# Performance work log

Measured on AMD Instinct MI355X. Metric: run time of the kernel, lower is better.

The kernel has to match this reference:

```python
import jax, jax.numpy as jnp
import numpy as np

D_MODEL = 1024
N_HEADS = 16
HEAD_DIM = D_MODEL // N_HEADS
D_FF = 4096
ROPE_BASE = 10000.0
LN_EPS = 1e-5


def setup_inputs() -> dict:
    key = jax.random.key(0)
    ks = jax.random.split(key, 12)
    B, S = 2, 2048
    s = 0.02
    inp = {
        "x": jax.random.normal(ks[0], (B, S, D_MODEL), dtype=jnp.float32),
        "Wq": jax.random.normal(ks[1], (D_MODEL, D_MODEL), dtype=jnp.float32) * s,
        "bq": jnp.zeros((D_MODEL,), jnp.float32),
        "Wk": jax.random.normal(ks[2], (D_MODEL, D_MODEL), dtype=jnp.float32) * s,
        "bk": jnp.zeros((D_MODEL,), jnp.float32),
        "Wv": jax.random.normal(ks[3], (D_MODEL, D_MODEL), dtype=jnp.float32) * s,
        "bv": jnp.zeros((D_MODEL,), jnp.float32),
        "Wo": jax.random.normal(ks[4], (D_MODEL, D_MODEL), dtype=jnp.float32) * s,
        "bo": jnp.zeros((D_MODEL,), jnp.float32),
        "ln1_g": jnp.ones((D_MODEL,), jnp.float32),
        "ln1_b": jnp.zeros((D_MODEL,), jnp.float32),
        "W1": jax.random.normal(ks[5], (D_MODEL, D_FF), dtype=jnp.float32) * s,
        "b1": jnp.zeros((D_FF,), jnp.float32),
        "W2": jax.random.normal(ks[6], (D_FF, D_MODEL), dtype=jnp.float32) * s,
        "b2": jnp.zeros((D_MODEL,), jnp.float32),
        "ln2_g": jnp.ones((D_MODEL,), jnp.float32),
        "ln2_b": jnp.zeros((D_MODEL,), jnp.float32),
    }
    return inp


def _layernorm(x, g, b):
    mu = jnp.mean(x, axis=-1, keepdims=True)
    var = jnp.var(x, axis=-1, keepdims=True)
    return (x - mu) * jax.lax.rsqrt(var + LN_EPS) * g + b


def _rope_cos_sin(seq_len, dtype):
    inv_freq = 1.0 / (ROPE_BASE ** (jnp.arange(0, HEAD_DIM, 2, dtype=jnp.float32) / HEAD_DIM))
    t = jnp.arange(seq_len, dtype=jnp.float32)
    freqs = jnp.einsum("i,j->ij", t, inv_freq)          # [S, HEAD_DIM/2]
    emb = jnp.concatenate([freqs, freqs], axis=-1)        # [S, HEAD_DIM]
    return jnp.cos(emb).astype(dtype), jnp.sin(emb).astype(dtype)


def _rotate_half(x):
    x1, x2 = jnp.split(x, 2, axis=-1)
    return jnp.concatenate([-x2, x1], axis=-1)


def reference(x, Wq, bq, Wk, bk, Wv, bv, Wo, bo, ln1_g, ln1_b,
              W1, b1, W2, b2, ln2_g, ln2_b):
    B, S, _ = x.shape
    residual = x
    h = _layernorm(x, ln1_g, ln1_b)

    def split_heads(y):  # [B,S,D] -> [B,H,S,hd]
        return y.reshape(B, S, N_HEADS, HEAD_DIM).transpose(0, 2, 1, 3)

    q = split_heads(h @ Wq + bq)
    k = split_heads(h @ Wk + bk)
    v = split_heads(h @ Wv + bv)

    cos, sin = _rope_cos_sin(S, x.dtype)  # [S, hd], broadcast over B,H
    q = q * cos + _rotate_half(q) * sin
    k = k * cos + _rotate_half(k) * sin

    scale = HEAD_DIM ** -0.5
    scores = jnp.einsum("bhqd,bhkd->bhqk", q, k) * scale
    attn = jax.nn.softmax(scores, axis=-1)
    ctx = jnp.einsum("bhqk,bhkd->bhqd", attn, v)           # [B,H,S,hd]
    ctx = ctx.transpose(0, 2, 1, 3).reshape(B, S, D_MODEL)
    attn_out = ctx @ Wo + bo

    x = residual + attn_out
    residual = x
    h = _layernorm(x, ln2_g, ln2_b)
    ffn = jax.nn.gelu(h @ W1 + b1, approximate=False) @ W2 + b2
    return residual + ffn
```

## Files before the change

### kernel.cpp

```cpp
#include <hip/hip_runtime.h>
#include <hip/hip_bf16.h>
#include <stdint.h>

#define S_LEN 2048
#define NH 16
#define HD 64
#define DM 1024
#define DFF 4096
#define MTOK 4096

typedef __attribute__((ext_vector_type(8))) short short8;
typedef __attribute__((ext_vector_type(4))) float f32x4;
typedef __attribute__((ext_vector_type(16))) float f32x16;
typedef __attribute__((ext_vector_type(2))) int i32x2;
typedef unsigned short u16;
typedef unsigned int u32;

__device__ __forceinline__ float bf2f(u16 u) {
  union { u32 i; float f; } x; x.i = ((u32)u) << 16; return x.f;
}
__device__ __forceinline__ u16 f2bf(float f) {
  union { float f; u32 i; } x; x.f = f;
  u32 r = x.i + 0x7fffu + ((x.i >> 16) & 1u);
  return (u16)(r >> 16);
}
__device__ __forceinline__ float exp2_fast(float x) {
  union { int i; float f; } u;
  u.i = (int)__builtin_fmaf(x, 8388608.0f, 1064986823.0f);
  return u.f;
}
__device__ __forceinline__ void gload16(const u16* g, u16* l) {
  __builtin_amdgcn_global_load_lds(
      (__attribute__((address_space(1))) u32*)g,
      (__attribute__((address_space(3))) u32*)l, 16, 0, 0);
}

#define VM0 asm volatile("s_waitcnt vmcnt(0)" ::: "memory")
#define BARR do { __builtin_amdgcn_s_barrier(); asm volatile("" ::: "memory"); } while (0)
#define LGKM0 do { asm volatile("s_waitcnt lgkmcnt(0)" ::: "memory"); __builtin_amdgcn_sched_barrier(0); } while (0)
#define PRIO1 __builtin_amdgcn_s_setprio(1)
#define PRIO0 __builtin_amdgcn_s_setprio(0)

__device__ __forceinline__ void transpose_tile(const float* __restrict__ W,
                                               u16* __restrict__ Wt, int K, int N,
                                               int n0, int k0, int tx, int ty,
                                               float (*tile)[33]) {
#pragma unroll
  for (int i = 0; i < 4; ++i)
    tile[ty + i * 8][tx] = W[(size_t)(k0 + ty + i * 8) * N + n0 + tx];
  __syncthreads();
#pragma unroll
  for (int i = 0; i < 4; ++i)
    Wt[(size_t)(n0 + ty + i * 8) * K + k0 + tx] = f2bf(tile[tx][ty + i * 8]);
}

__global__ __launch_bounds__(256) void prep(
    const float* __restrict__ Wq, const float* __restrict__ Wk,
    const float* __restrict__ Wv, const float* __restrict__ Wo,
    const float* __restrict__ W1, const float* __restrict__ W2,
    u16* __restrict__ WQKVT, u16* __restrict__ WOT, u16* __restrict__ W1T,
    u16* __restrict__ W2T, float* __restrict__ cosT, float* __restrict__ sinT,
    const float* __restrict__ x, const float* __restrict__ g,
    const float* __restrict__ b, u16* __restrict__ H) {
  __shared__ float tile[32][33];
  __shared__ float red[8];
  const int r = blockIdx.x;
  const int t = threadIdx.x;
  const int tx = t & 31, ty = t >> 5;
  if (r < 4096) {
    const float* W = (r < 1024) ? Wq : (r < 2048) ? Wk : (r < 3072) ? Wv : Wo;
    u16* Wt = (r < 1024) ? WQKVT
              : (r < 2048) ? WQKVT + 1024 * 1024
              : (r < 3072) ? WQKVT + 2 * 1024 * 1024 : WOT;
    int sub = r & 1023;
    transpose_tile(W, Wt, 1024, 1024, (sub & 31) * 32, (sub >> 5) * 32, tx, ty, tile);
  } else if (r < 8192) {
    int sub = r - 4096;
    transpose_tile(W1, W1T, 1024, 4096, (sub & 127) * 32, (sub >> 7) * 32, tx, ty, tile);
  } else if (r < 12288) {
    int sub = r - 8192;
    transpose_tile(W2, W2T, 4096, 1024, (sub & 31) * 32, (sub >> 5) * 32, tx, ty, tile);
  } else if (r < 12544) {
    int id = (r - 12288) * 256 + t;
    int s = id >> 5, j = id & 31;
    float inv = powf(10000.0f, -(float)j * (1.0f / 32.0f));
    float fr = (float)s * inv;
    cosT[id] = cosf(fr);
    sinT[id] = sinf(fr);
  } else {
    int row = r - 12544;
    float4 v = ((const float4*)(x + ((size_t)row << 10)))[t];
    float s = v.x + v.y + v.z + v.w;
    float q = v.x * v.x + v.y * v.y + v.z * v.z + v.w * v.w;
#pragma unroll
    for (int m = 1; m < 64; m <<= 1) {
      s += __shfl_xor(s, m, 64);
      q += __shfl_xor(q, m, 64);
    }
    int lane = t & 63, w = t >> 6;
    if (lane == 0) { red[w] = s; red[4 + w] = q; }
    __syncthreads();
    s = red[0] + red[1] + red[2] + red[3];
    q = red[4] + red[5] + red[6] + red[7];
    float mu = s * (1.0f / 1024.0f);
    float var = q * (1.0f / 1024.0f) - mu * mu;
    float rstd = rsqrtf(var + 1e-5f);
    float4 gv = ((const float4*)g)[t];
    float4 bv = ((const float4*)b)[t];
    ushort4 o;
    o.x = f2bf((v.x - mu) * rstd * gv.x + bv.x);
    o.y = f2bf((v.y - mu) * rstd * gv.y + bv.y);
    o.z = f2bf((v.z - mu) * rstd * gv.z + bv.z);
    o.w = f2bf((v.w - mu) * rstd * gv.w + bv.w);
    ((ushort4*)(H + ((size_t)row << 10)))[t] = o;
  }
}

__global__ __launch_bounds__(256) void ln_bf16(const float* __restrict__ x,
                                               const float* __restrict__ g,
                                               const float* __restrict__ b,
                                               u16* __restrict__ out) {
  int row = blockIdx.x;
  int t = threadIdx.x;
  float4 v = ((const float4*)(x + ((size_t)row << 10)))[t];
  float s = v.x + v.y + v.z + v.w;
  float q = v.x * v.x + v.y * v.y + v.z * v.z + v.w * v.w;
#pragma unroll
  for (int m = 1; m < 64; m <<= 1) {
    s += __shfl_xor(s, m, 64);
    q += __shfl_xor(q, m, 64);
  }
  __shared__ float red[8];
  int lane = t & 63, w = t >> 6;
  if (lane == 0) { red[w] = s; red[4 + w] = q; }
  __syncthreads();
  s = red[0] + red[1] + red[2] + red[3];
  q = red[4] + red[5] + red[6] + red[7];
  float mu = s * (1.0f / 1024.0f);
  float var = q * (1.0f / 1024.0f) - mu * mu;
  float rstd = rsqrtf(var + 1e-5f);
  float4 gv = ((const float4*)g)[t];
  float4 bv = ((const float4*)b)[t];
  ushort4 o;
  o.x = f2bf((v.x - mu) * rstd * gv.x + bv.x);
  o.y = f2bf((v.y - mu) * rstd * gv.y + bv.y);
  o.z = f2bf((v.z - mu) * rstd * gv.z + bv.z);
  o.w = f2bf((v.w - mu) * rstd * gv.w + bv.w);
  ((ushort4*)(out + ((size_t)row << 10)))[t] = o;
}

#define MMQ(IB, NB)                                                          \
  _Pragma("unroll") for (int i_ = 0; i_ < 4; ++i_)                           \
  _Pragma("unroll") for (int n_ = 0; n_ < 2; ++n_)                           \
  _Pragma("unroll") for (int k_ = 0; k_ < 2; ++k_)                           \
    acc[(IB) + i_][(NB) + n_] = __builtin_amdgcn_mfma_f32_16x16x32_bf16(     \
        a[i_][k_], b[(NB) + n_][k_], acc[(IB) + i_][(NB) + n_], 0, 0, 0);

template <int EPI>
__global__ __launch_bounds__(512, 2) void gemm256(
    const u16* __restrict__ A, const u16* __restrict__ Bt, int N, int K,
    const float* __restrict__ bias, const float* __restrict__ bq,
    const float* __restrict__ bk, const float* __restrict__ bv,
    const float* __restrict__ cosT, const float* __restrict__ sinT,
    u16* __restrict__ d0, u16* __restrict__ d1, u16* __restrict__ d2) {
  __shared__ __align__(16) u16 As[2][256 * 64];
  __shared__ __align__(16) u16 Bs[2][256 * 64];
  const int t = threadIdx.x;
  const int lane = t & 63, wid = t >> 6;
  const int fr = lane & 15, fq = lane >> 4;
  const int m0 = blockIdx.y << 8, n0 = blockIdx.x << 8;
  const int wmo = (wid >> 2) << 7;
  const int wno = (wid & 3) << 6;
  const int r7 = fr & 7;
  const int srow = t >> 3, ssl = t & 7;

  f32x4 acc[8][4];
#pragma unroll
  for (int i = 0; i < 8; ++i)
#pragma unroll
    for (int n = 0; n < 4; ++n) acc[i][n] = (f32x4){0.f, 0.f, 0.f, 0.f};

  short8 a[4][2], b[4][2];

  auto stageA = [&](int slot, int kt) {
#pragma unroll
    for (int c = 0; c < 4; ++c) {
      const int row = (c << 6) + srow;
      gload16(A + (size_t)(m0 + row) * K + kt + ((ssl ^ (row & 7)) << 3),
              &As[slot][(size_t)((c << 9) + t) << 3]);
    }
  };
  auto stageB = [&](int slot, int kt) {
#pragma unroll
    for (int c = 0; c < 4; ++c) {
      const int row = (c << 6) + srow;
      gload16(Bt + (size_t)(n0 + row) * K + kt + ((ssl ^ (row & 7)) << 3),
              &Bs[slot][(size_t)((c << 9) + t) << 3]);
    }
  };
  auto readA = [&](int slot, int ibase) {
#pragma unroll
    for (int i = 0; i < 4; ++i) {
      const u16* rp = &As[slot][(wmo + ((ibase + i) << 4) + fr) << 6];
      a[i][0] = *(const short8*)(rp + ((fq ^ r7) << 3));
      a[i][1] = *(const short8*)(rp + (((4 + fq) ^ r7) << 3));
    }
  };
  auto readB = [&](int slot, int nbase) {
#pragma unroll
    for (int n = 0; n < 2; ++n) {
      const u16* rp = &Bs[slot][(wno + ((nbase + n) << 4) + fr) << 6];
      b[nbase + n][0] = *(const short8*)(rp + ((fq ^ r7) << 3));
      b[nbase + n][1] = *(const short8*)(rp + (((4 + fq) ^ r7) << 3));
    }
  };

  stageA(0, 0);
  stageB(0, 0);
  const int iters = K >> 7;
  for (int it = 0; it < iters; ++it) {
    const int kt = it << 7;
    VM0; BARR;
    readA(0, 0); readB(0, 0);
    stageA(1, kt + 64);
    LGKM0; PRIO1; MMQ(0, 0); PRIO0;
    BARR;
    readB(0, 2);
    stageB(1, kt + 64);
    LGKM0; PRIO1; MMQ(0, 2); PRIO0;
    BARR;
    readA(0, 4);
    LGKM0; PRIO1; MMQ(4, 2); PRIO0;
    BARR;
    PRIO1; MMQ(4, 0); PRIO0;
    VM0; BARR;
    readA(1, 0); readB(1, 0);
    if (it + 1 < iters) stageA(0, kt + 128);
    LGKM0; PRIO1; MMQ(0, 0); PRIO0;
    BARR;
    readB(1, 2);
    if (it + 1 < iters) stageB(0, kt + 128);
    LGKM0; PRIO1; MMQ(0, 2); PRIO0;
    BARR;
    readA(1, 4);
    LGKM0; PRIO1; MMQ(4, 2); PRIO0;
    BARR;
    PRIO1; MMQ(4, 0); PRIO0;
  }

  if (EPI == 0) {
    const int colbase = n0 + wno;
    const int slice = colbase >> 10;
    const int cb = colbase & 1023;
    const int hh = cb >> 6;
    if (slice < 2) {
      const float sc = (slice == 0) ? 0.125f * 1.44269504088896f : 1.0f;
      const float* bb_ = (slice == 0) ? bq : bk;
      u16* dst = (slice == 0) ? d0 : d1;
#pragma unroll
      for (int i = 0; i < 8; ++i) {
        const int row0 = m0 + wmo + (i << 4) + (fq << 2);
#pragma unroll
        for (int n = 0; n < 2; ++n) {
          const int d = n * 16 + fr;
          const float blo = bb_[cb + d];
          const float bhi = bb_[cb + d + 32];
#pragma unroll
          for (int j = 0; j < 4; ++j) {
            const int row = row0 + j;
            const int ss = row & 2047, bb2 = row >> 11;
            const float c = cosT[ss * 32 + d];
            const float sn = sinT[ss * 32 + d];
            const float av = acc[i][n][j] + blo;
            const float bv2 = acc[i][n + 2][j] + bhi;
            const size_t base = ((size_t)((bb2 * 16 + hh) * 2048 + ss)) << 6;
            dst[base + d] = f2bf((av * c - bv2 * sn) * sc);
            dst[base + d + 32] = f2bf((bv2 * c + av * sn) * sc);
          }
        }
      }
    } else {
#pragma unroll
      for (int i = 0; i < 8; ++i) {
        const int row0 = m0 + wmo + (i << 4) + (fq << 2);
#pragma unroll
        for (int n = 0; n < 4; ++n) {
          const int d = n * 16 + fr;
          const float bia = bv[cb + d];
#pragma unroll
          for (int j = 0; j < 4; ++j) {
            const int row = row0 + j;
            const int ss = row & 2047, bb2 = row >> 11;
            d2[((size_t)((bb2 * 16 + hh) * 64 + d)) * 2048 + ss] =
                f2bf(acc[i][n][j] + bia);
          }
        }
      }
    }
  } else {
#pragma unroll
    for (int i = 0; i < 8; ++i) {
      const int row0 = m0 + wmo + (i << 4) + (fq << 2);
#pragma unroll
      for (int n = 0; n < 4; ++n) {
        const int col = n0 + wno + n * 16 + fr;
        const float bia = bias[col];
#pragma unroll
        for (int j = 0; j < 4; ++j) {
          const int row = row0 + j;
          const float v = acc[i][n][j] + bia;
          const float gl = 0.5f * v * (1.0f + erff(v * 0.70710678118f));
          d0[(size_t)row * N + col] = f2bf(gl);
        }
      }
    }
  }
}

__global__ __launch_bounds__(512, 1) void gemm_split(
    const u16* __restrict__ A, const u16* __restrict__ Bt, int K,
    const float* __restrict__ bias, const float* __restrict__ resid,
    float* __restrict__ dst) {
  __shared__ __align__(16) u16 As[2][128 * 128];
  __shared__ __align__(16) u16 Bs[2][128 * 128];
  const int t = threadIdx.x, lane = t & 63, w = t >> 6;
  const int fr = lane & 15, fq = lane >> 4;
  const int wq = w & 3, kh = w >> 2;
  const int wm = (wq >> 1) << 6, wn = (wq & 1) << 6;
  const int bid = blockIdx.x;
  const int xcd = bid & 7, within = bid >> 3;
  const int m0 = (xcd * 4 + (within >> 3)) << 7;
  const int n0 = (within & 7) << 7;
  const int srow = t >> 4;
  const int ssl = t & 15;

  f32x4 acc[4][4];
#pragma unroll
  for (int i = 0; i < 4; ++i)
#pragma unroll
    for (int n = 0; n < 4; ++n) acc[i][n] = (f32x4){0.f, 0.f, 0.f, 0.f};

  auto stage = [&](int buf, int kt) {
#pragma unroll
    for (int c = 0; c < 4; ++c) {
      const int R = c * 32 + srow;
      const int gs = ssl ^ (R & 15);
      gload16(A + (size_t)(m0 + R) * K + kt + gs * 8, &As[buf][R * 128 + ssl * 8]);
    }
#pragma unroll
    for (int c = 0; c < 4; ++c) {
      const int R = c * 32 + srow;
      const int gs = ssl ^ (R & 15);
      gload16(Bt + (size_t)(n0 + R) * K + kt + gs * 8, &Bs[buf][R * 128 + ssl * 8]);
    }
  };

  stage(0, 0);
  int buf = 0;
  const int iters = K >> 7;
  for (int it = 0; it < iters; ++it) {
    VM0;
    BARR;
    if (it + 1 < iters) stage(buf ^ 1, (it + 1) << 7);

    short8 a[4][2], b[4][2];
#pragma unroll
    for (int i = 0; i < 4; ++i) {
      const u16* rp = &As[buf][(wm + i * 16 + fr) * 128];
#pragma unroll
      for (int ks = 0; ks < 2; ++ks)
        a[i][ks] = *(const short8*)(rp + (((kh * 8 + ks * 4 + fq) ^ fr) << 3));
    }
#pragma unroll
    for (int n = 0; n < 4; ++n) {
      const u16* rp = &Bs[buf][(wn + n * 16 + fr) * 128];
#pragma unroll
      for (int ks = 0; ks < 2; ++ks)
        b[n][ks] = *(const short8*)(rp + (((kh * 8 + ks * 4 + fq) ^ fr) << 3));
    }
    PRIO1;
#pragma unroll
    for (int i = 0; i < 4; ++i)
#pragma unroll
      for (int n = 0; n < 4; ++n)
#pragma unroll
        for (int ks = 0; ks < 2; ++ks)
          acc[i][n] = __builtin_amdgcn_mfma_f32_16x16x32_bf16(a[i][ks], b[n][ks],
                                                              acc[i][n], 0, 0, 0);
    PRIO0;
    buf ^= 1;
  }

  BARR;
  float* mrg = (float*)&As[0][0];
  if (kh == 1) {
#pragma unroll
    for (int i = 0; i < 4; ++i) {
      const int ri = i * 16 + (fq << 2);
#pragma unroll
      for (int n = 0; n < 4; ++n) {
        const int ci = n * 16 + fr;
        *(f32x4*)(mrg + wq * 4352 + ci * 68 + ri) = acc[i][n];
      }
    }
  }
  LGKM0;
  BARR;
  if (kh == 0) {
#pragma unroll
    for (int i = 0; i < 4; ++i) {
      const int ri = i * 16 + (fq << 2);
      const int row0 = m0 + wm + ri;
#pragma unroll
      for (int n = 0; n < 4; ++n) {
        const int ci = n * 16 + fr;
        const int col = n0 + wn + ci;
        const f32x4 other = *(const f32x4*)(mrg + wq * 4352 + ci * 68 + ri);
        const float bia = bias[col];
#pragma unroll
        for (int j = 0; j < 4; ++j) {
          size_t idx = (size_t)(row0 + j) * 1024 + col;
          dst[idx] = acc[i][n][j] + other[j] + bia + resid[idx];
        }
      }
    }
  }
}

__global__ __launch_bounds__(512, 4) void attn_fwd(const u16* __restrict__ q,
                                                   const u16* __restrict__ k,
                                                   const u16* __restrict__ vt,
                                                   u16* __restrict__ ctx) {
  __shared__ __align__(16) u16 Ks[2][2][64 * 64];
  __shared__ __align__(16) u16 Vs[2][2][64 * 64];
  __shared__ float Lr[4][32];
  const int t = threadIdx.x, lane = t & 63, w = t >> 6;
  const int qsub = w & 3, half = w >> 2;
  const int ql = lane & 31;
  const int h = lane >> 5;
  const int bid = blockIdx.x;
  const int bh = (bid & 7) * 4 + ((bid >> 3) & 3);
  const int qt = bid >> 5;
  const int q0w = qt * 128 + qsub * 32;
  const size_t hbase = (size_t)bh << 17;
  const u16* kg = k + hbase;
  const u16* vg = vt + hbase;
  const int srow = t >> 3;
  const int sl = t & 7;
  const int l7 = lane & 7;

  short8 qf[4];
#pragma unroll
  for (int f = 0; f < 4; ++f)
    qf[f] = *(const short8*)(q + hbase + (size_t)(q0w + ql) * 64 + f * 16 + h * 8);

  float la[4] = {0.f, 0.f, 0.f, 0.f};
  f32x16 o[2];
#pragma unroll
  for (int db = 0; db < 2; ++db)
#pragma unroll
    for (int r = 0; r < 16; ++r) o[db][r] = 0.f;

  auto stage = [&](int buf, int it1) {
    const int kt0 = it1 << 6;
    const int kt1 = (16 + it1) << 6;
    const int gs = sl ^ (srow & 7);
    gload16(kg + (size_t)(kt0 + srow) * 64 + gs * 8, &Ks[0][buf][srow * 64 + sl * 8]);
    gload16(kg + (size_t)(kt1 + srow) * 64 + gs * 8, &Ks[1][buf][srow * 64 + sl * 8]);
    gload16(vg + (size_t)srow * 2048 + kt0 + gs * 8, &Vs[0][buf][srow * 64 + sl * 8]);
    gload16(vg + (size_t)srow * 2048 + kt1 + gs * 8, &Vs[1][buf][srow * 64 + sl * 8]);
  };

  stage(0, 0);
  int buf = 0;
  for (int it = 0; it < 16; ++it) {
    VM0;
    BARR;
    if (it < 15) stage(buf ^ 1, it + 1);

    f32x16 s[2];
    PRIO1;
#pragma unroll
    for (int kb = 0; kb < 2; ++kb) {
#pragma unroll
      for (int r = 0; r < 16; ++r) s[kb][r] = 0.f;
#pragma unroll
      for (int f = 0; f < 4; ++f) {
        const u16* kr = &Ks[half][buf][(kb * 32 + ql) * 64 + (((2 * f + h) ^ l7) << 3)];
        s[kb] = __builtin_amdgcn_mfma_f32_32x32x16_bf16(*(const short8*)kr, qf[f],
                                                        s[kb], 0, 0, 0);
      }
    }
    PRIO0;

    float p[2][16];
#pragma unroll
    for (int kb = 0; kb < 2; ++kb)
#pragma unroll
      for (int r = 0; r < 16; ++r) {
        p[kb][r] = exp2_fast(s[kb][r]);
        la[r & 3] += p[kb][r];
      }

    short8 pf[4];
#pragma unroll
    for (int kb = 0; kb < 2; ++kb)
#pragma unroll
      for (int rrp = 0; rrp < 2; ++rrp) {
        u32 y0, y1, x0, x1;
        asm volatile("v_cvt_pk_bf16_f32 %0, %1, %2" : "=v"(y0)
                     : "v"(p[kb][8 * rrp + 0]), "v"(p[kb][8 * rrp + 1]));
        asm volatile("v_cvt_pk_bf16_f32 %0, %1, %2" : "=v"(y1)
                     : "v"(p[kb][8 * rrp + 2]), "v"(p[kb][8 * rrp + 3]));
        asm volatile("v_cvt_pk_bf16_f32 %0, %1, %2" : "=v"(x0)
                     : "v"(p[kb][8 * rrp + 4]), "v"(p[kb][8 * rrp + 5]));
        asm volatile("v_cvt_pk_bf16_f32 %0, %1, %2" : "=v"(x1)
                     : "v"(p[kb][8 * rrp + 6]), "v"(p[kb][8 * rrp + 7]));
        i32x2 r0 = __builtin_amdgcn_permlane32_swap((int)x0, (int)y0, false, false);
        i32x2 r1 = __builtin_amdgcn_permlane32_swap((int)x1, (int)y1, false, false);
        u32 dw[4] = {(u32)r0[1], (u32)r1[1], (u32)r0[0], (u32)r1[0]};
        pf[kb * 2 + rrp] = *(short8*)dw;
      }

    PRIO1;
#pragma unroll
    for (int db = 0; db < 2; ++db) {
#pragma unroll
      for (int f = 0; f < 4; ++f) {
        const u16* vr = &Vs[half][buf][(db * 32 + ql) * 64 + (((2 * f + h) ^ l7) << 3)];
        o[db] = __builtin_amdgcn_mfma_f32_32x32x16_bf16(pf[f], *(const short8*)vr,
                                                        o[db], 0, 0, 0);
      }
    }
    PRIO0;
    buf ^= 1;
  }

  float lacc = (la[0] + la[1]) + (la[2] + la[3]);
  lacc += __shfl_xor(lacc, 32, 64);

  BARR;
  float* mO = (float*)&Ks[0][0][0];
  float* mL = (float*)&Vs[0][0][0];
  if (half == 1) {
#pragma unroll
    for (int r = 0; r < 16; ++r) {
      const int qr = (r & 3) + 8 * (r >> 2) + 4 * h;
#pragma unroll
      for (int db = 0; db < 2; ++db)
        mO[(qsub * 32 + qr) * 64 + db * 32 + ql] = o[db][r];
    }
    if (h == 0) mL[qsub * 32 + ql] = lacc;
  }
  LGKM0;
  BARR;
  if (half == 0) {
    float lsum = lacc + mL[qsub * 32 + ql];
    Lr[qsub][ql] = 1.0f / lsum;
#pragma unroll
    for (int r = 0; r < 16; ++r) {
      const int qr = (r & 3) + 8 * (r >> 2) + 4 * h;
#pragma unroll
      for (int db = 0; db < 2; ++db)
        o[db][r] += mO[(qsub * 32 + qr) * 64 + db * 32 + ql];
    }
    LGKM0;
    const int bb = bh >> 4, hh = bh & 15;
#pragma unroll
    for (int r = 0; r < 16; ++r) {
      const int qr = (r & 3) + 8 * (r >> 2) + 4 * h;
      const float rl = Lr[qsub][qr];
      const int row = q0w + qr;
      const size_t base = (((size_t)(bb * 2048 + row)) << 10) + hh * 64;
#pragma unroll
      for (int db = 0; db < 2; ++db)
        ctx[base + db * 32 + ql] = f2bf(o[db][r] * rl);
    }
  }
}

extern "C" void kernel_launch(void* const* d_in, const int* in_sizes, int n_in,
                              void* d_out, int out_size, void* d_ws, size_t ws_size,
                              hipStream_t stream) {
  const float* x    = (const float*)d_in[0];
  const float* Wq   = (const float*)d_in[1];
  const float* bq   = (const float*)d_in[2];
  const float* Wk   = (const float*)d_in[3];
  const float* bk   = (const float*)d_in[4];
  const float* Wv   = (const float*)d_in[5];
  const float* bv   = (const float*)d_in[6];
  const float* Wo   = (const float*)d_in[7];
  const float* bo   = (const float*)d_in[8];
  const float* ln1g = (const float*)d_in[9];
  const float* ln1b = (const float*)d_in[10];
  const float* W1   = (const float*)d_in[11];
  const float* b1   = (const float*)d_in[12];
  const float* W2   = (const float*)d_in[13];
  const float* b2   = (const float*)d_in[14];
  const float* ln2g = (const float*)d_in[15];
  const float* ln2b = (const float*)d_in[16];

  char* ws = (char*)d_ws;
  size_t off = 0;
  auto alloc = [&](size_t bytes) {
    char* p = ws + off;
    off += (bytes + 1023) & ~(size_t)1023;
    return p;
  };
  u16* WQKVT = (u16*)alloc((size_t)3 * DM * DM * 2);
  u16* WOT = (u16*)alloc((size_t)DM * DM * 2);
  u16* W1T = (u16*)alloc((size_t)DFF * DM * 2);
  u16* W2T = (u16*)alloc((size_t)DM * DFF * 2);
  float* COS = (float*)alloc((size_t)S_LEN * 32 * 4);
  float* SIN = (float*)alloc((size_t)S_LEN * 32 * 4);
  u16* H   = (u16*)alloc((size_t)MTOK * DM * 2);
  u16* Qb  = (u16*)alloc((size_t)MTOK * DM * 2);
  u16* Kb  = (u16*)alloc((size_t)MTOK * DM * 2);
  u16* VT  = (u16*)alloc((size_t)MTOK * DM * 2);
  u16* CTX = (u16*)alloc((size_t)MTOK * DM * 2);
  float* X2 = (float*)alloc((size_t)MTOK * DM * 4);
  u16* FFN1 = Qb;
  if (ws_size < off) return;

  dim3 blk256(256);
  prep<<<dim3(16640), blk256, 0, stream>>>(Wq, Wk, Wv, Wo, W1, W2, WQKVT, WOT,
                                           W1T, W2T, COS, SIN, x, ln1g, ln1b, H);
  gemm256<0><<<dim3(12, 16), dim3(512), 0, stream>>>(
      H, WQKVT, 3072, 1024, nullptr, bq, bk, bv, COS, SIN, Qb, Kb, VT);
  attn_fwd<<<dim3(512), dim3(512), 0, stream>>>(Qb, Kb, VT, CTX);
  gemm_split<<<dim3(256), dim3(512), 0, stream>>>(CTX, WOT, 1024, bo, x, X2);
  ln_bf16<<<4096, blk256, 0, stream>>>(X2, ln2g, ln2b, H);
  gemm256<1><<<dim3(16, 16), dim3(512), 0, stream>>>(
      H, W1T, 4096, 1024, b1, nullptr, nullptr, nullptr, nullptr, nullptr,
      FFN1, nullptr, nullptr);
  gemm_split<<<dim3(256), dim3(512), 0, stream>>>(FFN1, W2T, 4096, b2, X2, (float*)d_out);
}
```

Baseline: 219.6 us.

## Restructure GEMM main loop into half-tile staged pipeline with partial vmcnt waits

Rewrites the 256x256 GEMM main loop so that global-to-LDS loads are issued in half-tile chunks spread across the four MFMA phases, prefetching two k-tiles ahead. A partial vmcnt(6) wait replaces the full drain. All eight A fragments are now read once per k-tile, and launch bounds drop to one block per CU so the doubled A register array fits. The aim is to hide global load latency and reduce stalls, at the cost of lower occupancy and more register pressure.

Result: no change. 220.2 us (+0.2%).

```diff
diff --git a/kernel.cpp b/kernel.cpp
--- a/kernel.cpp
+++ b/kernel.cpp
@@ -36,6 +36,7 @@
 }
 
 #define VM0 asm volatile("s_waitcnt vmcnt(0)" ::: "memory")
+#define VM6 asm volatile("s_waitcnt vmcnt(6)" ::: "memory")
 #define BARR do { __builtin_amdgcn_s_barrier(); asm volatile("" ::: "memory"); } while (0)
 #define LGKM0 do { asm volatile("s_waitcnt lgkmcnt(0)" ::: "memory"); __builtin_amdgcn_sched_barrier(0); } while (0)
 #define PRIO1 __builtin_amdgcn_s_setprio(1)
@@ -149,15 +150,15 @@
   ((ushort4*)(out + ((size_t)row << 10)))[t] = o;
 }
 
-#define MMQ(IB, NB)                                                          \
+#define MMQ4(IB, NB)                                                         \
   _Pragma("unroll") for (int i_ = 0; i_ < 4; ++i_)                           \
   _Pragma("unroll") for (int n_ = 0; n_ < 2; ++n_)                           \
   _Pragma("unroll") for (int k_ = 0; k_ < 2; ++k_)                           \
     acc[(IB) + i_][(NB) + n_] = __builtin_amdgcn_mfma_f32_16x16x32_bf16(     \
-        a[i_][k_], b[(NB) + n_][k_], acc[(IB) + i_][(NB) + n_], 0, 0, 0);
+        a[(IB) + i_][k_], b[(NB) + n_][k_], acc[(IB) + i_][(NB) + n_], 0, 0, 0);
 
 template <int EPI>
-__global__ __launch_bounds__(512, 2) void gemm256(
+__global__ __launch_bounds__(512, 1) void gemm256(
     const u16* __restrict__ A, const u16* __restrict__ Bt, int N, int K,
     const float* __restrict__ bias, const float* __restrict__ bq,
     const float* __restrict__ bk, const float* __restrict__ bv,
@@ -172,7 +173,9 @@
   const int wmo = (wid >> 2) << 7;
   const int wno = (wid & 3) << 6;
   const int r7 = fr & 7;
-  const int srow = t >> 3, ssl = t & 7;
+  const int ssl = t & 7;
+  const u16* Ap = A + (size_t)m0 * K;
+  const u16* Bp = Bt + (size_t)n0 * K;
 
   f32x4 acc[8][4];
 #pragma unroll
@@ -180,33 +183,25 @@
 #pragma unroll
     for (int n = 0; n < 4; ++n) acc[i][n] = (f32x4){0.f, 0.f, 0.f, 0.f};
 
-  short8 a[4][2], b[4][2];
-
-  auto stageA = [&](int slot, int kt) {
-#pragma unroll
-    for (int c = 0; c < 4; ++c) {
-      const int row = (c << 6) + srow;
-      gload16(A + (size_t)(m0 + row) * K + kt + ((ssl ^ (row & 7)) << 3),
-              &As[slot][(size_t)((c << 9) + t) << 3]);
+  short8 a[8][2], b[4][2];
+
+  auto stageH = [&](u16* dstSlot, const u16* src, int rowOff, int kt) {
+#pragma unroll
+    for (int c = 0; c < 2; ++c) {
+      const int R = rowOff + (c << 6) + (t >> 3);
+      gload16(src + (size_t)R * K + kt + ((ssl ^ (R & 7)) << 3),
+              dstSlot + (size_t)R * 64 + ssl * 8);
     }
   };
-  auto stageB = [&](int slot, int kt) {
-#pragma unroll
-    for (int c = 0; c < 4; ++c) {
-      const int row = (c << 6) + srow;
-      gload16(Bt + (size_t)(n0 + row) * K + kt + ((ssl ^ (row & 7)) << 3),
-              &Bs[slot][(size_t)((c << 9) + t) << 3]);
-    }
-  };
-  auto readA = [&](int slot, int ibase) {
-#pragma unroll
-    for (int i = 0; i < 4; ++i) {
-      const u16* rp = &As[slot][(wmo + ((ibase + i) << 4) + fr) << 6];
+  auto readAall = [&](int slot) {
+#pragma unroll
+    for (int i = 0; i < 8; ++i) {
+      const u16* rp = &As[slot][(wmo + (i << 4) + fr) << 6];
       a[i][0] = *(const short8*)(rp + ((fq ^ r7) << 3));
       a[i][1] = *(const short8*)(rp + (((4 + fq) ^ r7) << 3));
     }
   };
-  auto readB = [&](int slot, int nbase) {
+  auto readB2 = [&](int slot, int nbase) {
 #pragma unroll
     for (int n = 0; n < 2; ++n) {
       const u16* rp = &Bs[slot][(wno + ((nbase + n) << 4) + fr) << 6];
@@ -215,37 +210,36 @@
     }
   };
 
-  stageA(0, 0);
-  stageB(0, 0);
-  const int iters = K >> 7;
-  for (int it = 0; it < iters; ++it) {
-    const int kt = it << 7;
-    VM0; BARR;
-    readA(0, 0); readB(0, 0);
-    stageA(1, kt + 64);
-    LGKM0; PRIO1; MMQ(0, 0); PRIO0;
+  const int nt = K >> 6;
+  stageH(&As[0][0], Ap, 0, 0);
+  stageH(&As[0][0], Ap, 128, 0);
+  stageH(&Bs[0][0], Bp, 0, 0);
+  stageH(&Bs[0][0], Bp, 128, 0);
+  stageH(&As[1][0], Ap, 0, 64);
+  stageH(&As[1][0], Ap, 128, 64);
+  stageH(&Bs[1][0], Bp, 0, 64);
+
+  for (int tt = 0; tt < nt; ++tt) {
+    const int s = tt & 1;
+    const int kt1 = (tt + 1) << 6, kt2 = (tt + 2) << 6;
+    if (tt + 1 < nt) { VM6; } else { VM0; }
     BARR;
-    readB(0, 2);
-    stageB(1, kt + 64);
-    LGKM0; PRIO1; MMQ(0, 2); PRIO0;
+    readAall(s);
+    readB2(s, 0);
+    if (tt + 1 < nt) stageH(&Bs[s ^ 1][0], Bp, 128, kt1);
+    LGKM0;
+    PRIO1; MMQ4(0, 0); PRIO0;
     BARR;
-    readA(0, 4);
-    LGKM0; PRIO1; MMQ(4, 2); PRIO0;
+    readB2(s, 2);
+    if (tt + 2 < nt) stageH(&As[s][0], Ap, 0, kt2);
+    LGKM0;
+    PRIO1; MMQ4(0, 2); PRIO0;
     BARR;
-    PRIO1; MMQ(4, 0); PRIO0;
-    VM0; BARR;
-    readA(1, 0); readB(1, 0);
-    if (it + 1 < iters) stageA(0, kt + 128);
-    LGKM0; PRIO1; MMQ(0, 0); PRIO0;
+    if (tt + 2 < nt) stageH(&As[s][0], Ap, 128, kt2);
+    PRIO1; MMQ4(4, 2); PRIO0;
     BARR;
-    readB(1, 2);
-    if (it + 1 < iters) stageB(0, kt + 128);
-    LGKM0; PRIO1; MMQ(0, 2); PRIO0;
-    BARR;
-    readA(1, 4);
-    LGKM0; PRIO1; MMQ(4, 2); PRIO0;
-    BARR;
-    PRIO1; MMQ(4, 0); PRIO0;
+    if (tt + 2 < nt) stageH(&Bs[s][0], Bp, 0, kt2);
+    PRIO1; MMQ4(4, 0); PRIO0;
   }
 
   if (EPI == 0) {
```

## Replace 256x256 double-buffered GEMM with simple 128x128 single-buffered tile GEMM

Applied to the files above, without the earlier changes.

Swaps the 256x256-tile, 8-wave, double-buffered, phase-interleaved GEMM used for QKV projection and FFN1 for a 128x128-tile, 4-wave kernel with one LDS buffer and a plain sync-load-compute loop. Blocks are mapped to tiles with a swizzle to improve L2 locality. The intent is more blocks in flight: 768/1024 blocks and 3 per CU, instead of 192/256 blocks that underfill 256 CUs. The cost is losing load/compute overlap and getting lower operand reuse per tile.

Measured after the change: 216.1 us. About the same (-1.6%).

```diff
diff --git a/kernel.cpp b/kernel.cpp
--- a/kernel.cpp
+++ b/kernel.cpp
@@ -149,107 +149,71 @@
   ((ushort4*)(out + ((size_t)row << 10)))[t] = o;
 }
 
-#define MMQ(IB, NB)                                                          \
-  _Pragma("unroll") for (int i_ = 0; i_ < 4; ++i_)                           \
-  _Pragma("unroll") for (int n_ = 0; n_ < 2; ++n_)                           \
-  _Pragma("unroll") for (int k_ = 0; k_ < 2; ++k_)                           \
-    acc[(IB) + i_][(NB) + n_] = __builtin_amdgcn_mfma_f32_16x16x32_bf16(     \
-        a[i_][k_], b[(NB) + n_][k_], acc[(IB) + i_][(NB) + n_], 0, 0, 0);
-
 template <int EPI>
-__global__ __launch_bounds__(512, 2) void gemm256(
+__global__ __launch_bounds__(256, 3) void gemm128(
     const u16* __restrict__ A, const u16* __restrict__ Bt, int N, int K,
     const float* __restrict__ bias, const float* __restrict__ bq,
     const float* __restrict__ bk, const float* __restrict__ bv,
     const float* __restrict__ cosT, const float* __restrict__ sinT,
     u16* __restrict__ d0, u16* __restrict__ d1, u16* __restrict__ d2) {
-  __shared__ __align__(16) u16 As[2][256 * 64];
-  __shared__ __align__(16) u16 Bs[2][256 * 64];
+  __shared__ __align__(16) u16 As[128 * 64];
+  __shared__ __align__(16) u16 Bs[128 * 64];
   const int t = threadIdx.x;
   const int lane = t & 63, wid = t >> 6;
   const int fr = lane & 15, fq = lane >> 4;
-  const int m0 = blockIdx.y << 8, n0 = blockIdx.x << 8;
-  const int wmo = (wid >> 2) << 7;
-  const int wno = (wid & 3) << 6;
   const int r7 = fr & 7;
+  const int bid = blockIdx.x;
+  const int mt = (bid & 7) * 4 + ((bid >> 3) & 3);
+  const int ntl = bid >> 5;
+  const int m0 = mt << 7, n0 = ntl << 7;
+  const int wm = (wid >> 1) << 6, wn = (wid & 1) << 6;
   const int srow = t >> 3, ssl = t & 7;
 
-  f32x4 acc[8][4];
-#pragma unroll
-  for (int i = 0; i < 8; ++i)
+  f32x4 acc[4][4];
+#pragma unroll
+  for (int i = 0; i < 4; ++i)
 #pragma unroll
     for (int n = 0; n < 4; ++n) acc[i][n] = (f32x4){0.f, 0.f, 0.f, 0.f};
 
-  short8 a[4][2], b[4][2];
-
-  auto stageA = [&](int slot, int kt) {
+  for (int kt = 0; kt < K; kt += 64) {
+    __syncthreads();
 #pragma unroll
     for (int c = 0; c < 4; ++c) {
-      const int row = (c << 6) + srow;
-      gload16(A + (size_t)(m0 + row) * K + kt + ((ssl ^ (row & 7)) << 3),
-              &As[slot][(size_t)((c << 9) + t) << 3]);
-    }
-  };
-  auto stageB = [&](int slot, int kt) {
-#pragma unroll
-    for (int c = 0; c < 4; ++c) {
-      const int row = (c << 6) + srow;
-      gload16(Bt + (size_t)(n0 + row) * K + kt + ((ssl ^ (row & 7)) << 3),
-              &Bs[slot][(size_t)((c << 9) + t) << 3]);
-    }
-  };
-  auto readA = [&](int slot, int ibase) {
+      const int R = (c << 5) + srow;
+      const int gs = ssl ^ (R & 7);
+      gload16(A + (size_t)(m0 + R) * K + kt + gs * 8, As + R * 64 + ssl * 8);
+      gload16(Bt + (size_t)(n0 + R) * K + kt + gs * 8, Bs + R * 64 + ssl * 8);
+    }
+    __syncthreads();
+    short8 a[4][2], b[4][2];
 #pragma unroll
     for (int i = 0; i < 4; ++i) {
-      const u16* rp = &As[slot][(wmo + ((ibase + i) << 4) + fr) << 6];
-      a[i][0] = *(const short8*)(rp + ((fq ^ r7) << 3));
-      a[i][1] = *(const short8*)(rp + (((4 + fq) ^ r7) << 3));
-    }
-  };
-  auto readB = [&](int slot, int nbase) {
-#pragma unroll
-    for (int n = 0; n < 2; ++n) {
-      const u16* rp = &Bs[slot][(wno + ((nbase + n) << 4) + fr) << 6];
-      b[nbase + n][0] = *(const short8*)(rp + ((fq ^ r7) << 3));
-      b[nbase + n][1] = *(const short8*)(rp + (((4 + fq) ^ r7) << 3));
-    }
-  };
-
-  stageA(0, 0);
-  stageB(0, 0);
-  const int iters = K >> 7;
-  for (int it = 0; it < iters; ++it) {
-    const int kt = it << 7;
-    VM0; BARR;
-    readA(0, 0); readB(0, 0);
-    stageA(1, kt + 64);
-    LGKM0; PRIO1; MMQ(0, 0); PRIO0;
-    BARR;
-    readB(0, 2);
-    stageB(1, kt + 64);
-    LGKM0; PRIO1; MMQ(0, 2); PRIO0;
-    BARR;
-    readA(0, 4);
-    LGKM0; PRIO1; MMQ(4, 2); PRIO0;
-    BARR;
-    PRIO1; MMQ(4, 0); PRIO0;
-    VM0; BARR;
-    readA(1, 0); readB(1, 0);
-    if (it + 1 < iters) stageA(0, kt + 128);
-    LGKM0; PRIO1; MMQ(0, 0); PRIO0;
-    BARR;
-    readB(1, 2);
-    if (it + 1 < iters) stageB(0, kt + 128);
-    LGKM0; PRIO1; MMQ(0, 2); PRIO0;
-    BARR;
-    readA(1, 4);
-    LGKM0; PRIO1; MMQ(4, 2); PRIO0;
-    BARR;
-    PRIO1; MMQ(4, 0); PRIO0;
+      const u16* rp = &As[(wm + i * 16 + fr) * 64];
+#pragma unroll
+      for (int ks = 0; ks < 2; ++ks)
+        a[i][ks] = *(const short8*)(rp + (((ks * 4 + fq) ^ r7) << 3));
+    }
+#pragma unroll
+    for (int n = 0; n < 4; ++n) {
+      const u16* rp = &Bs[(wn + n * 16 + fr) * 64];
+#pragma unroll
+      for (int ks = 0; ks < 2; ++ks)
+        b[n][ks] = *(const short8*)(rp + (((ks * 4 + fq) ^ r7) << 3));
+    }
+    PRIO1;
+#pragma unroll
+    for (int i = 0; i < 4; ++i)
+#pragma unroll
+      for (int n = 0; n < 4; ++n)
+#pragma unroll
+        for (int ks = 0; ks < 2; ++ks)
+          acc[i][n] = __builtin_amdgcn_mfma_f32_16x16x32_bf16(a[i][ks], b[n][ks],
+                                                              acc[i][n], 0, 0, 0);
+    PRIO0;
   }
 
   if (EPI == 0) {
-    const int colbase = n0 + wno;
+    const int colbase = n0 + wn;
     const int slice = colbase >> 10;
     const int cb = colbase & 1023;
     const int hh = cb >> 6;
@@ -258,8 +222,8 @@
       const float* bb_ = (slice == 0) ? bq : bk;
       u16* dst = (slice == 0) ? d0 : d1;
 #pragma unroll
-      for (int i = 0; i < 8; ++i) {
-        const int row0 = m0 + wmo + (i << 4) + (fq << 2);
+      for (int i = 0; i < 4; ++i) {
+        const int row0 = m0 + wm + i * 16 + (fq << 2);
 #pragma unroll
         for (int n = 0; n < 2; ++n) {
           const int d = n * 16 + fr;
@@ -281,8 +245,8 @@
       }
     } else {
 #pragma unroll
-      for (int i = 0; i < 8; ++i) {
-        const int row0 = m0 + wmo + (i << 4) + (fq << 2);
+      for (int i = 0; i < 4; ++i) {
+        const int row0 = m0 + wm + i * 16 + (fq << 2);
 #pragma unroll
         for (int n = 0; n < 4; ++n) {
           const int d = n * 16 + fr;
@@ -299,11 +263,11 @@
     }
   } else {
 #pragma unroll
-    for (int i = 0; i < 8; ++i) {
-      const int row0 = m0 + wmo + (i << 4) + (fq << 2);
+    for (int i = 0; i < 4; ++i) {
+      const int row0 = m0 + wm + i * 16 + (fq << 2);
 #pragma unroll
       for (int n = 0; n < 4; ++n) {
-        const int col = n0 + wno + n * 16 + fr;
+        const int col = n0 + wn + n * 16 + fr;
         const float bia = bias[col];
 #pragma unroll
         for (int j = 0; j < 4; ++j) {
@@ -625,12 +589,12 @@
   dim3 blk256(256);
   prep<<<dim3(16640), blk256, 0, stream>>>(Wq, Wk, Wv, Wo, W1, W2, WQKVT, WOT,
                                            W1T, W2T, COS, SIN, x, ln1g, ln1b, H);
-  gemm256<0><<<dim3(12, 16), dim3(512), 0, stream>>>(
+  gemm128<0><<<dim3(768), blk256, 0, stream>>>(
       H, WQKVT, 3072, 1024, nullptr, bq, bk, bv, COS, SIN, Qb, Kb, VT);
   attn_fwd<<<dim3(512), dim3(512), 0, stream>>>(Qb, Kb, VT, CTX);
   gemm_split<<<dim3(256), dim3(512), 0, stream>>>(CTX, WOT, 1024, bo, x, X2);
   ln_bf16<<<4096, blk256, 0, stream>>>(X2, ln2g, ln2b, H);
-  gemm256<1><<<dim3(16, 16), dim3(512), 0, stream>>>(
+  gemm128<1><<<dim3(1024), blk256, 0, stream>>>(
       H, W1T, 4096, 1024, b1, nullptr, nullptr, nullptr, nullptr, nullptr,
       FFN1, nullptr, nullptr);
   gemm_split<<<dim3(256), dim3(512), 0, stream>>>(FFN1, W2T, 4096, b2, X2, (float*)d_out);
```
